# Optimization experiments

Measured on AMD Instinct MI355X. Metric: run time of the kernel, lower is better.

## Reference

```python
import jax, jax.numpy as jnp
import numpy as np

B, L = 2, 2048
D_MODEL = 512
KERNEL = 5
DILATIONS = (1, 2, 4, 8, 1, 2, 4, 8)
HEADS = len(DILATIONS)
HEAD_W = D_MODEL // HEADS
MODE = "center"


def _dilocal_content(x_bedl, kernel, dilations, mode):
    # x_bedl: (B, E, D, L). Returns content in layout (B, L, E, H, K, D),
    # matching LCSA's dilocal + transpose(-4,-1).transpose(-4,-2).transpose(-5,-4).
    Lx = x_bedl.shape[-1]
    per_head = []
    for d in dilations:
        P = (kernel - 1) * d
        if mode == "forward":
            pads = (P, 0)
        elif mode == "backward":
            pads = (0, P)
        else:  # center
            pads = (P // 2, P - P // 2)
        padded = jnp.pad(x_bedl, ((0, 0),) * (x_bedl.ndim - 1) + (pads,))
        win = jnp.stack([padded[..., k * d:k * d + Lx] for k in range(kernel)], axis=-2)
        per_head.append(win)
    c = jnp.stack(per_head, axis=-2)  # (B, E, D, K, H, L)
    return jnp.transpose(c, (0, 5, 1, 4, 3, 2))  # (B, L, E, H, K, D)


def setup_inputs() -> dict:
    key = jax.random.key(0)
    ks = jax.random.split(key, 6)
    s_in = 1.0 / np.sqrt(D_MODEL)
    s_out = 1.0 / np.sqrt(HEADS * HEAD_W)
    x = jax.random.normal(ks[0], (B, L, D_MODEL), jnp.float32)
    q_w = jax.random.normal(ks[1], (1, HEADS, 1, HEAD_W, D_MODEL), jnp.float32) * s_in
    q_b = jnp.zeros((1, HEADS, 1, HEAD_W), jnp.float32)
    k_w = jax.random.normal(ks[2], (1, HEADS, KERNEL, HEAD_W, D_MODEL), jnp.float32) * s_in
    k_b = jnp.zeros((1, HEADS, KERNEL, HEAD_W), jnp.float32)
    v_w = jax.random.normal(ks[3], (1, HEADS, KERNEL, HEAD_W, D_MODEL), jnp.float32) * s_in
    v_b = jnp.zeros((1, HEADS, KERNEL, HEAD_W), jnp.float32)
    o_w = jax.random.normal(ks[4], (1, D_MODEL, HEADS * HEAD_W), jnp.float32) * s_out
    o_b = jnp.zeros((1, D_MODEL), jnp.float32)
    return {"x": x, "q_w": q_w, "q_b": q_b, "k_w": k_w, "k_b": k_b,
            "v_w": v_w, "v_b": v_b, "o_w": o_w, "o_b": o_b}


def reference(x, q_w, q_b, k_w, k_b, v_w, v_b, o_w, o_b) -> jnp.ndarray:
    b, l, _ = x.shape
    # ensemble=None path: unsqueeze(-3) then transpose(-2,-1) -> (B, E=1, D, L)
    t = jnp.swapaxes(x[:, None, :, :], -2, -1)
    content = _dilocal_content(t, KERNEL, DILATIONS, MODE)  # (B, L, 1, H, K, D)
    # query uses kernel_width=1 (no padding, dilation irrelevant): (B, L, 1, H, 1, D)
    query = jnp.broadcast_to(x[:, :, None, None, None, :], (b, l, 1, HEADS, 1, D_MODEL))
    # per-(head, kernel-position) projections
    q = jnp.einsum('blehkd,ehkod->blehko', query, q_w) + q_b      # (B,L,1,H,1,O)
    k = jnp.einsum('blehkd,ehkod->blehko', content, k_w) + k_b    # (B,L,1,H,K,O)
    v = jnp.einsum('blehkd,ehkod->blehko', content, v_w) + v_b    # (B,L,1,H,K,O)
    logits = jnp.einsum('blehqo,blehko->blehqk', q, k)            # (B,L,1,H,1,K)
    score = jax.nn.softmax(logits, axis=-1)
    attn = jnp.einsum('blehqk,blehko->blehqo', score, v) / jnp.sqrt(jnp.float32(HEAD_W))
    attn = attn[..., 0, :]                                        # squeeze(-2) -> (B,L,1,H,O)
    flat = attn.reshape(b, l, 1, HEADS * HEAD_W)
    out = jnp.einsum('blef,eof->bleo', flat, o_w) + o_b           # (B,L,1,D)
    # transpose(-3,-2) then squeeze ensemble -> (B, L, D)
    return out[:, :, 0, :]
```

## Files before the change

kernel.cpp:

```cpp
#include <hip/hip_runtime.h>
#include <hip/hip_bf16.h>

using bf16 = __hip_bfloat16;
typedef __attribute__((ext_vector_type(8))) short short8;
typedef __attribute__((ext_vector_type(4))) float f32x4;
typedef __attribute__((ext_vector_type(16))) float f32x16;

__device__ __constant__ int c_dil[8] = {1, 2, 4, 8, 1, 2, 4, 8};

__device__ inline void store1(float* p, float v) { *p = v; }
__device__ inline void store1(bf16* p, float v) { *p = __float2bfloat16(v); }

__device__ inline void gload_lds16(const void* g, void* l) {
    __builtin_amdgcn_global_load_lds(
        (const __attribute__((address_space(1))) unsigned int*)g,
        (__attribute__((address_space(3))) unsigned int*)l, 16, 0, 0);
}

template <int N> __device__ inline void vwait() {
    asm volatile("s_waitcnt vmcnt(%0)" :: "n"(N) : "memory");
    __builtin_amdgcn_sched_barrier(0);
}
__device__ inline void barrier_pin() {
    __builtin_amdgcn_s_barrier();
    __builtin_amdgcn_sched_barrier(0);
}

__device__ inline unsigned short f2bf(float f) {
    const unsigned u = __float_as_uint(f);
    return (unsigned short)((u + 0x7fffu + ((u >> 16) & 1u)) >> 16);
}
__device__ inline float bf2f(unsigned short h) { return __uint_as_float(((unsigned)h) << 16); }

__device__ inline void conv_block(const float* __restrict__ src, bf16* __restrict__ dst,
                                  int ld, int mode, int idx) {
    const float4 v = *reinterpret_cast<const float4*>(src + idx);
    const int r = idx >> 9, c = idx & 511;
    bf16* d = dst + (size_t)r * ld + c;
    const float vv[4] = {v.x, v.y, v.z, v.w};
    ushort4 hi, lo;
    unsigned short* hp = &hi.x; unsigned short* lp = &lo.x;
#pragma unroll
    for (int j = 0; j < 4; ++j) {
        hp[j] = f2bf(vv[j]);
        lp[j] = f2bf(vv[j] - bf2f(hp[j]));
    }
    *reinterpret_cast<ushort4*>(d) = hi;
    if (mode == 1) *reinterpret_cast<ushort4*>(d + 512) = lo;
}

__global__ __launch_bounds__(256) void conv_all(
    const float* __restrict__ x,  const float* __restrict__ qw, const float* __restrict__ kw,
    const float* __restrict__ vw, const float* __restrict__ ow,
    const float* __restrict__ qb, const float* __restrict__ kb,
    bf16* A2, bf16* Wqk, bf16* Wv, bf16* Wo, float* bqk)
{
    const int b = blockIdx.x, t = threadIdx.x;
    if (b < 2048)       conv_block(x,  A2,                      1024, 1, (b * 256 + t) * 4);
    else if (b < 2304)  conv_block(qw, Wqk,                      512, 0, ((b - 2048) * 256 + t) * 4);
    else if (b < 3584)  conv_block(kw, Wqk + (size_t)512 * 512,  512, 0, ((b - 2304) * 256 + t) * 4);
    else if (b < 4864)  conv_block(vw, Wv,                       512, 0, ((b - 3584) * 256 + t) * 4);
    else if (b < 5120)  conv_block(ow, Wo,                       512, 0, ((b - 4864) * 256 + t) * 4);
    else { const int i = (b - 5120) * 256 + t; bqk[i] = (i < 512) ? qb[i] : kb[i - 512]; }
}

template <bool HILO>
__device__ __forceinline__ void run_gemm(
    short* smem,
    const bf16* __restrict__ A,
    const bf16* __restrict__ W,
    const float* __restrict__ bias,
    bf16* __restrict__ C, int ldc,
    int bm, int bn)
{
    constexpr int NSTEPS = 16;
    short* Ahi = smem;
    short* Alo = smem + 8192;
    short* Bs  = smem + 16384;

    const int tid = threadIdx.x, wid = tid >> 6, lane = tid & 63;

    const int sslot = (((tid & 3) ^ ((tid >> 3) & 3)) << 4);
    const char* pAh = (const char*)A + (size_t)(bm + (tid >> 2)) * 2048 + sslot;
    const char* pB0 = (const char*)W + (size_t)(bn + (tid >> 2)) * 1024 + sslot;

    auto stage = [&](int kt) {
        char* da = (char*)(Ahi + (kt & 1) * 4096);
        char* db = (char*)(Bs  + (kt & 1) * 8192);
        gload_lds16(pAh,          da + wid * 1024);
        gload_lds16(pAh + 131072, da + 4096 + wid * 1024);
        if (HILO) {
            char* dl = (char*)(Alo + (kt & 1) * 4096);
            gload_lds16(pAh + 1024,          dl + wid * 1024);
            gload_lds16(pAh + 1024 + 131072, dl + 4096 + wid * 1024);
        }
        gload_lds16(pB0,           db + wid * 1024);
        gload_lds16(pB0 + 65536,   db + 4096 + wid * 1024);
        gload_lds16(pB0 + 131072,  db + 8192 + wid * 1024);
        gload_lds16(pB0 + 196608,  db + 12288 + wid * 1024);
        pAh += 64; pB0 += 64;
    };

    f32x16 acc[2][4];
#pragma unroll
    for (int m = 0; m < 2; ++m)
#pragma unroll
        for (int n = 0; n < 4; ++n)
#pragma unroll
            for (int j = 0; j < 16; ++j) acc[m][n][j] = 0.f;

    const int l31  = lane & 31;
    const int khalf = lane >> 5;
    const int swz  = (l31 >> 1) & 3;
    const int k0   = ((khalf)     ^ swz) << 3;
    const int k1   = ((2 + khalf) ^ swz) << 3;
    const int wrM = wid >> 1, wcN = wid & 1;
    const int arow0 = wrM * 64 + l31;
    const int brow0 = wcN * 128 + l31;

    stage(0);

    for (int kt = 0; kt < NSTEPS; ++kt) {
        vwait<0>();
        barrier_pin();

        const short* ah = Ahi + (kt & 1) * 4096;
        const short* al = Alo + (kt & 1) * 4096;
        const short* bb = Bs  + (kt & 1) * 8192;
        short8 fh[2][2], fl[2][2], bw[2][4];
#pragma unroll
        for (int m = 0; m < 2; ++m) {
            fh[0][m] = *(const short8*)&ah[(arow0 + m * 32) * 32 + k0];
            fh[1][m] = *(const short8*)&ah[(arow0 + m * 32) * 32 + k1];
            if (HILO) {
                fl[0][m] = *(const short8*)&al[(arow0 + m * 32) * 32 + k0];
                fl[1][m] = *(const short8*)&al[(arow0 + m * 32) * 32 + k1];
            }
        }
#pragma unroll
        for (int n = 0; n < 4; ++n) {
            bw[0][n] = *(const short8*)&bb[(brow0 + n * 32) * 32 + k0];
            bw[1][n] = *(const short8*)&bb[(brow0 + n * 32) * 32 + k1];
        }

        if (kt + 1 < NSTEPS) stage(kt + 1);

        __builtin_amdgcn_s_setprio(1);
#pragma unroll
        for (int ks = 0; ks < 2; ++ks)
#pragma unroll
            for (int m = 0; m < 2; ++m)
#pragma unroll
                for (int n = 0; n < 4; ++n)
                    acc[m][n] = __builtin_amdgcn_mfma_f32_32x32x16_bf16(fh[ks][m], bw[ks][n], acc[m][n], 0, 0, 0);
        if (HILO) {
#pragma unroll
            for (int ks = 0; ks < 2; ++ks)
#pragma unroll
                for (int m = 0; m < 2; ++m)
#pragma unroll
                    for (int n = 0; n < 4; ++n)
                        acc[m][n] = __builtin_amdgcn_mfma_f32_32x32x16_bf16(fl[ks][m], bw[ks][n], acc[m][n], 0, 0, 0);
        }
        __builtin_amdgcn_s_setprio(0);
    }

    const int rb4 = 4 * khalf;
#pragma unroll
    for (int m = 0; m < 2; ++m) {
#pragma unroll
        for (int n = 0; n < 4; ++n) {
            const int col = bn + wcN * 128 + n * 32 + l31;
            const float bv = bias[col];
#pragma unroll
            for (int j = 0; j < 16; ++j) {
                const int row = bm + wrM * 64 + m * 32 + (j & 3) + 8 * (j >> 2) + rb4;
                store1(C + (size_t)row * ldc + col, acc[m][n][j] + bv);
            }
        }
    }
}

__global__ __launch_bounds__(256, 2) void gemm_qkv(
    const bf16* __restrict__ A,
    const bf16* __restrict__ Wqk, const float* __restrict__ bqk, bf16* __restrict__ PQK,
    const bf16* __restrict__ Wv,  const float* __restrict__ vb,  bf16* __restrict__ PV)
{
    __shared__ short smem[32768];
    const int b = blockIdx.x;
    if (b < 64) {
        const int xcd = b & 7, i = b >> 3;
        const int by = xcd * 4 + (i & 3), bx = i >> 2;
        run_gemm<true>(smem, A, Wqk, bqk, PQK, 3072, by * 128, bx * 256);
    } else if (b < 384) {
        const int v = b - 64;
        const int xcd = v & 7, i = v >> 3;
        const int by = xcd * 4 + (i & 3), bx = i >> 2;
        run_gemm<false>(smem, A, Wqk + (size_t)512 * 512, bqk + 512,
                        PQK + 512, 3072, by * 128, bx * 256);
    } else {
        const int v = b - 384;
        const int xcd = v & 7, i = v >> 3;
        const int by = xcd * 4 + (i & 3), bx = i >> 2;
        run_gemm<false>(smem, A, Wv, vb, PV, 2560, by * 128, bx * 256);
    }
}

template <int BN, typename TC>
__global__ __launch_bounds__(256) void gemm128(
    const bf16* __restrict__ A, int lda, int cw, int rpx,
    const bf16* __restrict__ W0, int ldw0, const float* __restrict__ b0,
    TC* __restrict__ C0, int ldc0, int nt0, int nx0)
{
    constexpr int NF = BN / 32;
    constexpr int NLOAD = (BN == 128) ? 4 : 3;
    __shared__ short As[4][128 * 32];
    __shared__ short Bs[4][BN * 32];

    const int tid = threadIdx.x, wid = tid >> 6, lane = tid & 63;

    const int xcd = (int)blockIdx.x & 7;
    const int i   = (int)blockIdx.x >> 3;
    const int grp = rpx * cw;
    const int cc = i / grp, w2 = i % grp;
    const int rr = w2 / cw, c = w2 % cw;
    const int bx = cc * cw + c;
    const int by = xcd * rpx + rr;

    const int bm = by * 128;
    const int bn = bx * BN;
    const int nsteps = nt0;

    const int srow = lane >> 2;
    const int ssw  = (((lane & 3) ^ ((lane >> 3) & 3)) << 4);
    const char* pA0 = (const char*)A + (size_t)(bm + wid * 16 + srow) * lda * 2 + ssw;
    const char* pA1 = pA0 + (size_t)64 * lda * 2;
    const char* pB0 = (const char*)W0 + (size_t)(bn + wid * 16 + srow) * ldw0 * 2 + ssw;

    f32x4 acc[4][NF];
#pragma unroll
    for (int m = 0; m < 4; ++m)
#pragma unroll
        for (int n = 0; n < NF; ++n) acc[m][n] = f32x4{0.f, 0.f, 0.f, 0.f};

    const int lr16 = lane & 15;
    const int wsw8 = (((lane >> 4) ^ ((lr16 >> 1) & 3)) << 3);
    const int wr = wid >> 1, wc = wid & 1;
    int offA[4], offB[NF];
#pragma unroll
    for (int m = 0; m < 4; ++m) offA[m] = (wr * 4 + m) * 512 + lr16 * 32 + wsw8;
#pragma unroll
    for (int n = 0; n < NF; ++n) offB[n] = (wc * NF + n) * 512 + lr16 * 32 + wsw8;

    auto stage = [&](int buf) {
        gload_lds16(pA0, (char*)As[buf] + wid * 1024);
        gload_lds16(pA1, (char*)As[buf] + (wid + 4) * 1024);
        gload_lds16(pB0, (char*)Bs[buf] + wid * 1024);
        pA0 += 64; pA1 += 64; pB0 += 64;
    };

    stage(0);
    stage(1);
    stage(2);

    for (int s = 0; s < nsteps; ++s) {
        const int cur = s & 3;
        if (s + 2 < nsteps)      vwait<2 * NLOAD>();
        else if (s + 1 < nsteps) vwait<NLOAD>();
        else                     vwait<0>();
        barrier_pin();

        if (s + 3 < nsteps) stage((s + 3) & 3);

        short8 af[4], bw[NF];
#pragma unroll
        for (int m = 0; m < 4; ++m)
            af[m] = *(const short8*)&As[cur][offA[m]];
#pragma unroll
        for (int n = 0; n < NF; ++n)
            bw[n] = *(const short8*)&Bs[cur][offB[n]];

        __builtin_amdgcn_s_setprio(1);
#pragma unroll
        for (int m = 0; m < 4; ++m)
#pragma unroll
            for (int n = 0; n < NF; ++n)
                acc[m][n] = __builtin_amdgcn_mfma_f32_16x16x32_bf16(af[m], bw[n], acc[m][n], 0, 0, 0);
        __builtin_amdgcn_s_setprio(0);
    }

    const int r4 = (lane >> 4) * 4;
#pragma unroll
    for (int m = 0; m < 4; ++m) {
#pragma unroll
        for (int n = 0; n < NF; ++n) {
            const int col = bn + wc * (NF * 16) + n * 16 + lr16;
            const float bv = b0[col];
#pragma unroll
            for (int jj = 0; jj < 4; ++jj) {
                const int row = bm + wr * 64 + m * 16 + r4 + jj;
                store1(C0 + (size_t)row * ldc0 + col, acc[m][n][jj] + bv);
            }
        }
    }
}

__global__ __launch_bounds__(256) void attn_k(
    const bf16* __restrict__ PQK, const bf16* __restrict__ PV, bf16* __restrict__ Aout)
{
    const int lane = threadIdx.x & 63;
    const int wave = threadIdx.x >> 6;
    const int bl = blockIdx.x * 4 + wave;
    const int l  = bl & 2047;
    const int h  = lane >> 3;
    const int d  = c_dil[h];
    const int o8 = (lane & 7) * 8;

    float q[8];
    {
        const short8 qv = *(const short8*)&PQK[(size_t)bl * 3072 + lane * 8];
#pragma unroll
        for (int i = 0; i < 8; ++i) q[i] = bf2f((unsigned short)qv[i]);
    }

    float logits[5];
    float vv[5][8];
#pragma unroll
    for (int kk = 0; kk < 5; ++kk) {
        const int pos = l + (kk - 2) * d;
        const bool ok = (pos >= 0) && (pos < 2048);
        float s = 0.f;
        if (ok) {
            const size_t rb = (size_t)(bl - l + pos);
            const int coff = h * 320 + kk * 64 + o8;
            const short8 kv = *(const short8*)&PQK[rb * 3072 + 512 + coff];
            const short8 vvv = *(const short8*)&PV[rb * 2560 + coff];
#pragma unroll
            for (int i = 0; i < 8; ++i) {
                s = fmaf(bf2f((unsigned short)kv[i]), q[i], s);
                vv[kk][i] = bf2f((unsigned short)vvv[i]);
            }
        } else {
#pragma unroll
            for (int i = 0; i < 8; ++i) vv[kk][i] = 0.f;
        }
        s += __shfl_xor(s, 1);
        s += __shfl_xor(s, 2);
        s += __shfl_xor(s, 4);
        logits[kk] = s;
    }

    float mx = logits[0];
#pragma unroll
    for (int kk = 1; kk < 5; ++kk) mx = fmaxf(mx, logits[kk]);
    float e[5], ssum = 0.f;
#pragma unroll
    for (int kk = 0; kk < 5; ++kk) { e[kk] = __expf(logits[kk] - mx); ssum += e[kk]; }
    const float sc = 0.125f / ssum;

    short8 outv;
#pragma unroll
    for (int i = 0; i < 8; ++i) {
        float a = 0.f;
#pragma unroll
        for (int kk = 0; kk < 5; ++kk) a = fmaf(e[kk], vv[kk][i], a);
        outv[i] = (short)f2bf(a * sc);
    }
    *(short8*)&Aout[(size_t)bl * 512 + lane * 8] = outv;
}

extern "C" void kernel_launch(void* const* d_in, const int* in_sizes, int n_in,
                              void* d_out, int out_size, void* d_ws, size_t ws_size,
                              hipStream_t stream)
{
    const float* x   = (const float*)d_in[0];
    const float* q_w = (const float*)d_in[1];
    const float* q_b = (const float*)d_in[2];
    const float* k_w = (const float*)d_in[3];
    const float* k_b = (const float*)d_in[4];
    const float* v_w = (const float*)d_in[5];
    const float* v_b = (const float*)d_in[6];
    const float* o_w = (const float*)d_in[7];
    const float* o_b = (const float*)d_in[8];
    float* out = (float*)d_out;

    const int M = 4096;

    char* p = (char*)d_ws;
    bf16* A2  = (bf16*)p;  p += (size_t)M * 1024 * 2;
    bf16* Wqk = (bf16*)p;  p += (size_t)3072 * 512 * 2;
    bf16* Wv  = (bf16*)p;  p += (size_t)2560 * 512 * 2;
    bf16* Wo  = (bf16*)p;  p += (size_t)512 * 512 * 2;
    float* bqk = (float*)p; p += 3072 * 4;
    bf16* PQK = (bf16*)p;  p += (size_t)M * 3072 * 2;
    bf16* PV  = (bf16*)p;
    bf16* Aout = A2;

    conv_all<<<dim3(5132), dim3(256), 0, stream>>>(x, q_w, k_w, v_w, o_w, q_b, k_b,
                                                   A2, Wqk, Wv, Wo, bqk);
    gemm_qkv<<<dim3(704), dim3(256), 0, stream>>>(A2, Wqk, bqk, PQK, Wv, v_b, PV);
    attn_k<<<dim3(2048), dim3(256), 0, stream>>>(PQK, PV, Aout);
    gemm128<64, float><<<dim3(256), dim3(256), 0, stream>>>(
        Aout, 512, 8, 4,
        Wo, 512, o_b, out, 512, 16, 8);
}
```

Measured before the change: 71.81 us.

## Use persistent atomic work queue for QKV GEMM tiles

The QKV projection GEMM now launches a fixed grid of 512 persistent workgroups (2 per CU on 256 CUs) instead of 704 one-shot blocks. Each workgroup repeatedly pulls a tile index from a global atomic counter, which the conversion kernel resets to zero. The goal is to balance the heavier hi/lo Q tiles against the plain K/V tiles and avoid a partial last wave. In exchange it adds atomic and barrier overhead per tile and drops the XCD-aware tile swizzle, which may reduce L2 reuse.

```diff
diff --git a/kernel.cpp b/kernel.cpp
--- a/kernel.cpp
+++ b/kernel.cpp
@@ -53,7 +53,7 @@
     const float* __restrict__ x,  const float* __restrict__ qw, const float* __restrict__ kw,
     const float* __restrict__ vw, const float* __restrict__ ow,
     const float* __restrict__ qb, const float* __restrict__ kb,
-    bf16* A2, bf16* Wqk, bf16* Wv, bf16* Wo, float* bqk)
+    bf16* A2, bf16* Wqk, bf16* Wv, bf16* Wo, float* bqk, int* counter)
 {
     const int b = blockIdx.x, t = threadIdx.x;
     if (b < 2048)       conv_block(x,  A2,                      1024, 1, (b * 256 + t) * 4);
@@ -61,7 +61,8 @@
     else if (b < 3584)  conv_block(kw, Wqk + (size_t)512 * 512,  512, 0, ((b - 2304) * 256 + t) * 4);
     else if (b < 4864)  conv_block(vw, Wv,                       512, 0, ((b - 3584) * 256 + t) * 4);
     else if (b < 5120)  conv_block(ow, Wo,                       512, 0, ((b - 4864) * 256 + t) * 4);
-    else { const int i = (b - 5120) * 256 + t; bqk[i] = (i < 512) ? qb[i] : kb[i - 512]; }
+    else if (b < 5132) { const int i = (b - 5120) * 256 + t; bqk[i] = (i < 512) ? qb[i] : kb[i - 512]; }
+    else if (t == 0)    *counter = 0;
 }
 
 template <bool HILO>
@@ -184,25 +185,32 @@
 __global__ __launch_bounds__(256, 2) void gemm_qkv(
     const bf16* __restrict__ A,
     const bf16* __restrict__ Wqk, const float* __restrict__ bqk, bf16* __restrict__ PQK,
-    const bf16* __restrict__ Wv,  const float* __restrict__ vb,  bf16* __restrict__ PV)
+    const bf16* __restrict__ Wv,  const float* __restrict__ vb,  bf16* __restrict__ PV,
+    int* __restrict__ counter)
 {
     __shared__ short smem[32768];
-    const int b = blockIdx.x;
-    if (b < 64) {
-        const int xcd = b & 7, i = b >> 3;
-        const int by = xcd * 4 + (i & 3), bx = i >> 2;
-        run_gemm<true>(smem, A, Wqk, bqk, PQK, 3072, by * 128, bx * 256);
-    } else if (b < 384) {
-        const int v = b - 64;
-        const int xcd = v & 7, i = v >> 3;
-        const int by = xcd * 4 + (i & 3), bx = i >> 2;
-        run_gemm<false>(smem, A, Wqk + (size_t)512 * 512, bqk + 512,
-                        PQK + 512, 3072, by * 128, bx * 256);
-    } else {
-        const int v = b - 384;
-        const int xcd = v & 7, i = v >> 3;
-        const int by = xcd * 4 + (i & 3), bx = i >> 2;
-        run_gemm<false>(smem, A, Wv, vb, PV, 2560, by * 128, bx * 256);
+    __shared__ int s_job;
+
+    for (;;) {
+        __syncthreads();
+        if (threadIdx.x == 0) s_job = atomicAdd(counter, 1);
+        __syncthreads();
+        const int job = s_job;
+        if (job >= 704) break;
+
+        if (job < 64) {
+            const int by = job >> 1, bx = job & 1;
+            run_gemm<true>(smem, A, Wqk, bqk, PQK, 3072, by * 128, bx * 256);
+        } else if (job < 384) {
+            const int t = job - 64;
+            const int by = t / 10, bx = t % 10;
+            run_gemm<false>(smem, A, Wqk + (size_t)512 * 512, bqk + 512,
+                            PQK + 512, 3072, by * 128, bx * 256);
+        } else {
+            const int t = job - 384;
+            const int by = t / 10, bx = t % 10;
+            run_gemm<false>(smem, A, Wv, vb, PV, 2560, by * 128, bx * 256);
+        }
     }
 }
 
@@ -393,12 +401,13 @@
     bf16* Wo  = (bf16*)p;  p += (size_t)512 * 512 * 2;
     float* bqk = (float*)p; p += 3072 * 4;
     bf16* PQK = (bf16*)p;  p += (size_t)M * 3072 * 2;
-    bf16* PV  = (bf16*)p;
+    bf16* PV  = (bf16*)p;  p += (size_t)M * 2560 * 2;
+    int* counter = (int*)p;
     bf16* Aout = A2;
 
-    conv_all<<<dim3(5132), dim3(256), 0, stream>>>(x, q_w, k_w, v_w, o_w, q_b, k_b,
-                                                   A2, Wqk, Wv, Wo, bqk);
-    gemm_qkv<<<dim3(704), dim3(256), 0, stream>>>(A2, Wqk, bqk, PQK, Wv, v_b, PV);
+    conv_all<<<dim3(5133), dim3(256), 0, stream>>>(x, q_w, k_w, v_w, o_w, q_b, k_b,
+                                                   A2, Wqk, Wv, Wo, bqk, counter);
+    gemm_qkv<<<dim3(512), dim3(256), 0, stream>>>(A2, Wqk, bqk, PQK, Wv, v_b, PV, counter);
     attn_k<<<dim3(2048), dim3(256), 0, stream>>>(PQK, PV, Aout);
     gemm128<64, float><<<dim3(256), dim3(256), 0, stream>>>(
         Aout, 512, 8, 4,
```

Result: slower. 81.40 us (+13.4%).
